# Performance work log

Hardware: AMD Instinct MI355X
Metric: run time of the kernel (lower is better)

The kernel has to match this reference:

```python
import jax, jax.numpy as jnp
import numpy as np

N_NODES = 10000
N_EDGES = 160000
C = 64        # latent channels
H = 512       # MLP hidden width
L = 2         # allegro layers
NB = 8        # bessel basis size
CUT = 2.0     # radial cutoff
AVG = 3.0     # avg_num_neighbors


def setup_inputs() -> dict:
    key = jax.random.key(0)
    ks = jax.random.split(key, 12)
    positions = jax.random.normal(ks[0], (N_NODES, 3), jnp.float32)
    species = jax.random.randint(ks[1], (N_NODES,), 0, 2, jnp.int32)
    senders = jax.random.randint(ks[2], (N_EDGES,), 0, N_NODES, jnp.int32)
    receivers = jax.random.randint(ks[3], (N_EDGES,), 0, N_NODES, jnp.int32)
    w = lambda k, shape, fan: (jax.random.normal(k, shape, jnp.float32) / np.sqrt(fan).astype(np.float32))
    return dict(
        positions=positions,
        W_emb1=w(ks[4], (NB + 4, H), NB + 4),
        W_emb2=w(ks[5], (H, C), H),
        W_v=w(ks[6], (C, C), C),
        W_env=w(ks[7], (L, C, C), C),
        W_lat1=w(ks[8], (L, 3 * C, H), 3 * C),
        W_lat2=w(ks[9], (L, H, C), H),
        W_mix=w(ks[10], (L, C, 2 * C), C),
        W_out=w(ks[11], (C,), C),
        species=species, senders=senders, receivers=receivers,
    )


def reference(positions, W_emb1, W_emb2, W_v, W_env, W_lat1, W_lat2, W_mix, W_out,
              species, senders, receivers):
    node_attrs = jax.nn.one_hot(species, 2, dtype=positions.dtype)   # [N,2]
    r = positions[receivers] - positions[senders]                    # [E,3] edge vectors ('1o')
    d = jnp.sqrt(jnp.sum(r * r, axis=-1))                            # [E]
    dsafe = jnp.maximum(d, 1e-6)
    u = r / dsafe[:, None]                                           # unit vectors = l=1 spherical harmonics

    # radial basis: Bessel functions with smooth polynomial cutoff envelope
    xc = d / CUT
    env = jnp.where(xc < 1.0, (1.0 - xc ** 2) ** 2, 0.0)             # [E]
    nvec = jnp.arange(1, NB + 1, dtype=positions.dtype)
    bessel = jnp.sqrt(2.0 / CUT) * jnp.sin(nvec * jnp.pi * xc[:, None]) / dsafe[:, None]
    rad = bessel * env[:, None]                                      # [E,NB]

    # two-body latent embedding
    feat = jnp.concatenate([rad, node_attrs[senders], node_attrs[receivers]], axis=-1)  # [E,NB+4]
    x = (jax.nn.silu(feat @ W_emb1) @ W_emb2) * env[:, None]         # [E,C]
    # initial equivariant edge features (C channels of 1o)
    V = (x @ W_v)[:, :, None] * u[:, None, :]                        # [E,C,3]

    inv_sqrt2 = 1.0 / jnp.sqrt(2.0)
    for l in range(L):
        # environment density: scatter edge basis to sender nodes, gather back per edge
        w_e = x @ W_env[l]                                           # [E,C]
        rho1 = jax.ops.segment_sum(w_e[:, :, None] * u[:, None, :], senders,
                                   num_segments=N_NODES) / AVG       # [N,C,3] (1o density)
        rho0 = jax.ops.segment_sum(w_e, senders, num_segments=N_NODES) / AVG  # [N,C] (0e density)
        rho1_e = rho1[senders]                                       # [E,C,3]
        rho0_e = rho0[senders]                                       # [E,C]

        # channel-wise Clebsch-Gordan tensor products (lmax=1 paths)
        tp_scal = jnp.einsum('eci,eci->ec', V, rho1_e)               # 1o x 1o -> 0e
        tp_vec1 = V * rho0_e[:, :, None]                             # 1o x 0e -> 1o
        tp_vec2 = jnp.cross(V, rho1_e)                               # 1o x 1o -> 1e

        # latent update (residual, envelope-gated)
        lat_in = jnp.concatenate([x, tp_scal, rho0_e], axis=-1)      # [E,3C]
        dx = (jax.nn.silu(lat_in @ W_lat1[l]) @ W_lat2[l]) * env[:, None]
        x = (x + dx) * inv_sqrt2

        # equivariant update: latent-conditioned mix of tensor-product outputs
        mix = x @ W_mix[l]                                           # [E,2C]
        V = mix[:, :C, None] * tp_vec1 + mix[:, C:, None] * tp_vec2  # [E,C,3]

    # per-edge scalar readout, scatter-reduced to nodes
    e_edge = (x @ W_out) * env                                       # [E]
    node_energy = jax.ops.segment_sum(e_edge, receivers, num_segments=N_NODES) / AVG
    return node_energy
```

## Files before the change

### kernel.cpp

```cpp
#include <hip/hip_runtime.h>
#include <hip/hip_bf16.h>

#define E_NUM 160000
#define NN 10000
#define PI_F 3.14159265358979323846f

using u16 = unsigned short;
using u32 = unsigned int;
typedef short bf16x8 __attribute__((ext_vector_type(8)));
typedef float f32x4 __attribute__((ext_vector_type(4)));
typedef u32 u32x4 __attribute__((ext_vector_type(4)));

__device__ __forceinline__ float silu_fast(float z) {
    return z * __builtin_amdgcn_rcpf(1.0f + __expf(-z));
}
__device__ __forceinline__ float bfb2f(u32 bits16) {
    return __builtin_bit_cast(float, bits16 << 16);
}
__device__ __forceinline__ u32 f2bfb(float f) {
    return (u32)__builtin_bit_cast(u16, __float2bfloat16(f));
}
__device__ __forceinline__ u32 pack2(float lo, float hi) {
    return f2bfb(lo) | (f2bfb(hi) << 16);
}

__global__ void k_detect(const u16* __restrict__ posraw, int* __restrict__ flag) {
    int i = blockIdx.x * 256 + threadIdx.x;
    if (i >= 15000) return;
    float v = bfb2f((u32)posraw[2 * i]);
    if (!(fabsf(v) < 1e4f)) atomicOr(flag, 1);
}

__global__ void k_cvt_all(const void* s0, const void* s1, const void* s2,
                          const void* s3, const void* s4, const void* s5,
                          const void* s6, const void* s7, const void* s8,
                          float* __restrict__ dst, const int* __restrict__ flag) {
    int i = blockIdx.x * 256 + threadIdx.x;
    if (i >= 359792) return;
    const void* src; int off;
    if      (i < 30000)  { src = s0; off = i; }
    else if (i < 36144)  { src = s1; off = i - 30000; }
    else if (i < 68912)  { src = s2; off = i - 36144; }
    else if (i < 73008)  { src = s3; off = i - 68912; }
    else if (i < 81200)  { src = s4; off = i - 73008; }
    else if (i < 277808) { src = s5; off = i - 81200; }
    else if (i < 343344) { src = s6; off = i - 277808; }
    else if (i < 359728) { src = s7; off = i - 343344; }
    else                 { src = s8; off = i - 359728; }
    if (*flag) dst[i] = ((const float*)src)[off];
    else       dst[i] = bfb2f((u32)((const u16*)src)[off]);
}

__global__ void k_pack(const float* __restrict__ W, int K, int Nshift,
                       u16* __restrict__ hi, u16* __restrict__ lo) {
    int i = blockIdx.x * 256 + threadIdx.x;
    int total = K << Nshift;
    if (i >= total) return;
    int k = i >> Nshift, n = i & ((1 << Nshift) - 1);
    float w = W[i];
    u16 h = (u16)f2bfb(w);
    float r = w - bfb2f((u32)h);
    int idx = ((((k >> 3) << Nshift) + n) << 3) + (k & 7);
    hi[idx] = h; lo[idx] = (u16)f2bfb(r);
}

__global__ void k_pack_emb1(const float* __restrict__ W , u16* __restrict__ pk) {
    int i = blockIdx.x * 256 + threadIdx.x;
    if (i >= 64 * 512) return;
    int k = i >> 9, n = i & 511;
    u16 out = 0;
    if (k < 24) {
        out = (u16)f2bfb(W[(k % 12) * 512 + n]);
    } else if (k < 36) {
        float w = W[(k - 24) * 512 + n];
        u16 h = (u16)f2bfb(w);
        out = (u16)f2bfb(w - bfb2f((u32)h));
    }
    pk[((((k >> 3) << 9) + n) << 3) + (k & 7)] = out;
}

__global__ void k_hist(const int* __restrict__ senders, int* __restrict__ counts) {
    int e = blockIdx.x * 256 + threadIdx.x;
    if (e < E_NUM) atomicAdd(&counts[senders[e]], 1);
}

__global__ __launch_bounds__(1024) void k_scan(const int* __restrict__ counts,
                                               int* __restrict__ rowstart) {
    __shared__ int part[1024];
    int t = threadIdx.x;
    int base = t * 10;
    int local[10];
    int sum = 0;
    #pragma unroll
    for (int i = 0; i < 10; i++) {
        int v = (base + i < NN) ? counts[base + i] : 0;
        local[i] = sum; sum += v;
    }
    part[t] = sum;
    __syncthreads();
    for (int off = 1; off < 1024; off <<= 1) {
        int v = (t >= off) ? part[t - off] : 0;
        __syncthreads();
        part[t] += v;
        __syncthreads();
    }
    int pre = (t == 0) ? 0 : part[t - 1];
    #pragma unroll
    for (int i = 0; i < 10; i++)
        if (base + i < NN) rowstart[base + i] = pre + local[i];
    if (t == 1023) rowstart[NN] = part[1023];
}

__global__ void k_copy_int(const int* __restrict__ src, int* __restrict__ dst, int n) {
    int i = blockIdx.x * 256 + threadIdx.x;
    if (i < n) dst[i] = src[i];
}

__global__ void k_fill(const int* __restrict__ senders, int* __restrict__ cursor,
                       int* __restrict__ edge_list) {
    int e = blockIdx.x * 256 + threadIdx.x;
    if (e >= E_NUM) return;
    int pos = atomicAdd(&cursor[senders[e]], 1);
    edge_list[pos] = e;
}

__global__ void k_geom(const float* __restrict__ posf, const int* __restrict__ species,
                       const int* __restrict__ senders, const int* __restrict__ receivers,
                       const int* __restrict__ edge_list,
                       int* __restrict__ ssend, int* __restrict__ srecv,
                       float* __restrict__ ux, float* __restrict__ uy, float* __restrict__ uz,
                       float* __restrict__ envb, u32* __restrict__ latin) {
    int e = blockIdx.x * 256 + threadIdx.x;
    if (e >= E_NUM) return;
    int orig = edge_list[e];
    int s = senders[orig], r = receivers[orig];
    ssend[e] = s; srecv[e] = r;
    float rx = posf[3 * r + 0] - posf[3 * s + 0];
    float ry = posf[3 * r + 1] - posf[3 * s + 1];
    float rz = posf[3 * r + 2] - posf[3 * s + 2];
    float d = sqrtf(rx * rx + ry * ry + rz * rz);
    float inv = 1.0f / fmaxf(d, 1e-6f);
    ux[e] = rx * inv; uy[e] = ry * inv; uz[e] = rz * inv;
    float xc = d * 0.5f;
    float env = 0.0f;
    if (xc < 1.0f) { float t = 1.0f - xc * xc; env = t * t; }
    envb[e] = env;
    float ft[12];
    float se = env * inv;
    #pragma unroll
    for (int n = 1; n <= 8; n++) ft[n - 1] = __sinf((float)n * PI_F * xc) * se;
    int ss = species[s], sr = species[r];
    ft[8] = (ss == 0) ? 1.0f : 0.0f;
    ft[9] = (ss == 1) ? 1.0f : 0.0f;
    ft[10] = (sr == 0) ? 1.0f : 0.0f;
    ft[11] = (sr == 1) ? 1.0f : 0.0f;
    u32 fh[12]; float fl[12];
    #pragma unroll
    for (int i = 0; i < 12; i++) {
        fh[i] = f2bfb(ft[i]);
        fl[i] = ft[i] - bfb2f(fh[i]);
    }
    #pragma unroll
    for (int j = 0; j < 6; j++) {
        u32 v = fh[2 * j] | (fh[2 * j + 1] << 16);
        latin[(size_t)j * E_NUM + e] = v;
        latin[(size_t)(12 + j) * E_NUM + e] = v;
        latin[(size_t)(6 + j) * E_NUM + e] = pack2(fl[2 * j], fl[2 * j + 1]);
    }
}

__global__ __launch_bounds__(256) void k_rho_gather(
    const float* __restrict__ we, const int* __restrict__ rowstart,
    const float* __restrict__ ux, const float* __restrict__ uy,
    const float* __restrict__ uz,
    float* __restrict__ rho0, float* __restrict__ rho1) {
    int wv = (blockIdx.x * 256 + threadIdx.x) >> 6;
    int c = threadIdx.x & 63;
    if (wv >= NN) return;
    int start = rowstart[wv], end = rowstart[wv + 1];
    float s0 = 0.0f, sx = 0.0f, sy = 0.0f, sz = 0.0f;
    for (int j = start; j < end; j++) {
        float w = we[(size_t)j * 64 + c];
        float a = ux[j], b = uy[j], g = uz[j];
        s0 += w;
        sx = fmaf(w, a, sx);
        sy = fmaf(w, b, sy);
        sz = fmaf(w, g, sz);
    }
    const float inv3 = 1.0f / 3.0f;
    rho0[(size_t)wv * 64 + c] = s0 * inv3;
    rho1[(size_t)wv * 192 + 3 * c + 0] = sx * inv3;
    rho1[(size_t)wv * 192 + 3 * c + 1] = sy * inv3;
    rho1[(size_t)wv * 192 + 3 * c + 2] = sz * inv3;
}

template<int KSTEPS, int MODE, int HASLO, int FUSEWE, int STAGE>
__global__ __launch_bounds__(512, 4) void k_mlp(
    const u32* __restrict__ latin,
    const u16* __restrict__ W1hi, const u16* __restrict__ W1lo,
    const u16* __restrict__ W2hi, const u16* __restrict__ W2lo,
    const float* __restrict__ envb,
    u16* __restrict__ xout,
    const u16* __restrict__ wehi, const u16* __restrict__ welo,
    float* __restrict__ webuf,
    const u16* __restrict__ xin,
    const u16* __restrict__ x0t,
    const int* __restrict__ ssend,
    const float* __restrict__ ux, const float* __restrict__ uy,
    const float* __restrict__ uz,
    const float* __restrict__ rho0A, const float* __restrict__ rho1A,
    const float* __restrict__ rho0B, const float* __restrict__ rho1B,
    const u16* __restrict__ wvhi, const u16* __restrict__ wvlo,
    const u16* __restrict__ wmhi, const u16* __restrict__ wmlo) {
    constexpr int ROWDW = KSTEPS * 16;
    constexpr int INAREG = 24576;
    constexpr int SMEMSZ = (STAGE == 2) ? (INAREG + 2 * 16640) : (INAREG + 16640);
    __shared__ __align__(16) char smem[SMEMSZ];
    u32* inA = (u32*)smem;
    u16* hA  = (u16*)(smem + INAREG);
    float* tbA = (float*)(smem + INAREG);
    u16* mb   = (u16*)(smem + INAREG + 16640);
    u32* mb32 = (u32*)(smem + INAREG + 16640);
    u32* xt0  = (u32*)(smem + INAREG + 16640);
    int lane = threadIdx.x & 63;
    int sub = threadIdx.x >> 6;
    int w = __builtin_amdgcn_readfirstlane(sub);
    int l15 = lane & 15, quad = lane >> 4;
    int e0 = blockIdx.x * 64;
    int e = e0 + lane;

    if (STAGE == 0) {
        constexpr int CPW = (KSTEPS * 4) / 8;
        #pragma unroll
        for (int j = 0; j < CPW; j++) {
            int c = w * CPW + j;
            u32x4 v;
            #pragma unroll
            for (int i = 0; i < 4; i++) v[i] = latin[(size_t)(c * 4 + i) * E_NUM + e];
            int slot = (c & ~7) | ((c ^ lane) & 7);
            *(u32x4*)(&inA[lane * ROWDW + slot * 4]) = v;
        }
        __syncthreads();
    } else {
        {
            int c = w;
            u32x4 v;
            #pragma unroll
            for (int i = 0; i < 4; i++) {
                u32 lo = (u32)xin[(size_t)(8 * c + 2 * i) * E_NUM + e];
                u32 hi = (u32)xin[(size_t)(8 * c + 2 * i + 1) * E_NUM + e];
                v[i] = lo | (hi << 16);
            }
            int slot = (c & ~7) | ((c ^ lane) & 7);
            *(u32x4*)(&inA[lane * ROWDW + slot * 4]) = v;
        }
        if (STAGE == 2) {
            int c = w;
            u32x4 v;
            #pragma unroll
            for (int i = 0; i < 4; i++) {
                u32 lo = (u32)x0t[(size_t)(8 * c + 2 * i) * E_NUM + e];
                u32 hi = (u32)x0t[(size_t)(8 * c + 2 * i + 1) * E_NUM + e];
                v[i] = lo | (hi << 16);
            }
            int slot = (c ^ lane) & 7;
            *(u32x4*)(&xt0[lane * 32 + slot * 4]) = v;
        }
        __syncthreads();
        int mt = w & 3;
        int ntbA = (w >> 2) * 2;
        f32x4 accA[2];
        accA[0] = (f32x4){0.f, 0.f, 0.f, 0.f};
        accA[1] = (f32x4){0.f, 0.f, 0.f, 0.f};
        #pragma unroll
        for (int ks = 0; ks < 2; ks++) {
            int c = ks * 4 + quad;
            int m = mt * 16 + l15;
            bf16x8 af;
            if (STAGE == 1) {
                int slot = (c & ~7) | ((c ^ m) & 7);
                af = *(const bf16x8*)(&inA[m * ROWDW + slot * 4]);
            } else {
                int slot = (c ^ m) & 7;
                af = *(const bf16x8*)(&xt0[m * 32 + slot * 4]);
            }
            #pragma unroll
            for (int nti = 0; nti < 2; nti++) {
                int n = (ntbA + nti) * 16 + l15;
                size_t bidx = (((size_t)c << 6) + n) << 3;
                bf16x8 bh = *(const bf16x8*)(wvhi + bidx);
                accA[nti] = __builtin_amdgcn_mfma_f32_16x16x32_bf16(af, bh, accA[nti], 0, 0, 0);
                bf16x8 bl = *(const bf16x8*)(wvlo + bidx);
                accA[nti] = __builtin_amdgcn_mfma_f32_16x16x32_bf16(af, bl, accA[nti], 0, 0, 0);
            }
        }
        f32x4 accM[4];
        if (STAGE == 2) {
            #pragma unroll
            for (int i = 0; i < 4; i++) accM[i] = (f32x4){0.f, 0.f, 0.f, 0.f};
            int nbM = (w >> 2) * 4;
            #pragma unroll
            for (int ks = 0; ks < 2; ks++) {
                int c = ks * 4 + quad;
                int m = mt * 16 + l15;
                int slot = (c & ~7) | ((c ^ m) & 7);
                bf16x8 af = *(const bf16x8*)(&inA[m * ROWDW + slot * 4]);
                #pragma unroll
                for (int nti = 0; nti < 4; nti++) {
                    int n = (nbM + nti) * 16 + l15;
                    size_t bidx = (((size_t)c << 7) + n) << 3;
                    bf16x8 bh = *(const bf16x8*)(wmhi + bidx);
                    accM[nti] = __builtin_amdgcn_mfma_f32_16x16x32_bf16(af, bh, accM[nti], 0, 0, 0);
                    bf16x8 bl = *(const bf16x8*)(wmlo + bidx);
                    accM[nti] = __builtin_amdgcn_mfma_f32_16x16x32_bf16(af, bl, accM[nti], 0, 0, 0);
                }
            }
        }
        __syncthreads();
        #pragma unroll
        for (int nti = 0; nti < 2; nti++) {
            #pragma unroll
            for (int r = 0; r < 4; r++) {
                int rowD = mt * 16 + quad * 4 + r;
                int colD = (ntbA + nti) * 16 + l15;
                tbA[colD * 65 + rowD] = accA[nti][r];
            }
        }
        if (STAGE == 2) {
            int sel = (w >= 4) ? 1 : 0;
            #pragma unroll
            for (int nti = 0; nti < 4; nti++) {
                #pragma unroll
                for (int r = 0; r < 4; r++) {
                    int rowD = mt * 16 + quad * 4 + r;
                    int colD = nti * 16 + l15;
                    mb[((colD * 65 + rowD) << 1) + sel] = (u16)f2bfb(accM[nti][r]);
                }
            }
        }
        __syncthreads();
        int c0 = w * 8;
        float av[8], m1v[8], m2v[8];
        #pragma unroll
        for (int i = 0; i < 8; i++) av[i] = tbA[(c0 + i) * 65 + lane];
        if (STAGE == 2) {
            #pragma unroll
            for (int i = 0; i < 8; i++) {
                u32 pv = mb32[(c0 + i) * 65 + lane];
                m1v[i] = bfb2f(pv & 0xffffu);
                m2v[i] = bfb2f(pv >> 16);
            }
        }
        int s = ssend[e];
        float u0 = ux[e], u1 = uy[e], u2 = uz[e];
        float ts[8], rr[8];
        if (STAGE == 1) {
            const float* r1 = rho1A + (size_t)s * 192;
            const float* r0 = rho0A + (size_t)s * 64;
            #pragma unroll
            for (int i = 0; i < 8; i++) {
                int c = c0 + i;
                float dot = u0 * r1[3 * c] + u1 * r1[3 * c + 1] + u2 * r1[3 * c + 2];
                ts[i] = av[i] * dot;
                rr[i] = r0[c];
            }
        } else {
            const float* r1A = rho1A + (size_t)s * 192;
            const float* r0A = rho0A + (size_t)s * 64;
            const float* r1B = rho1B + (size_t)s * 192;
            const float* r0B = rho0B + (size_t)s * 64;
            #pragma unroll
            for (int i = 0; i < 8; i++) {
                int c = c0 + i;
                float v0 = av[i] * u0, v1 = av[i] * u1, v2 = av[i] * u2;
                float aA0 = r1A[3 * c], aA1 = r1A[3 * c + 1], aA2 = r1A[3 * c + 2];
                float rc = r0A[c];
                float w0 = m1v[i] * v0 * rc + m2v[i] * (v1 * aA2 - v2 * aA1);
                float w1 = m1v[i] * v1 * rc + m2v[i] * (v2 * aA0 - v0 * aA2);
                float w2 = m1v[i] * v2 * rc + m2v[i] * (v0 * aA1 - v1 * aA0);
                ts[i] = w0 * r1B[3 * c] + w1 * r1B[3 * c + 1] + w2 * r1B[3 * c + 2];
                rr[i] = r0B[c];
            }
        }
        u32x4 tv, rv;
        #pragma unroll
        for (int j = 0; j < 4; j++) {
            tv[j] = pack2(ts[2 * j], ts[2 * j + 1]);
            rv[j] = pack2(rr[2 * j], rr[2 * j + 1]);
        }
        {
            int c = 8 + w;
            int slot = (c & ~7) | ((c ^ lane) & 7);
            *(u32x4*)(&inA[lane * ROWDW + slot * 4]) = tv;
        }
        {
            int c = 16 + w;
            int slot = (c & ~7) | ((c ^ lane) & 7);
            *(u32x4*)(&inA[lane * ROWDW + slot * 4]) = rv;
        }
        __syncthreads();
    }

    f32x4 acc2[2];
    acc2[0] = (f32x4){0.f, 0.f, 0.f, 0.f};
    acc2[1] = (f32x4){0.f, 0.f, 0.f, 0.f};
    int nt2 = w & 3;
    int mt2a = (w >> 2) * 2;

    #pragma unroll
    for (int hh = 0; hh < 4; hh++) {
        f32x4 acc[4];
        #pragma unroll
        for (int mt = 0; mt < 4; mt++) acc[mt] = (f32x4){0.f, 0.f, 0.f, 0.f};
        #pragma unroll
        for (int ks = 0; ks < KSTEPS; ks++) {
            int c = ks * 4 + quad;
            bf16x8 afr[4];
            #pragma unroll
            for (int mt = 0; mt < 4; mt++) {
                int m = mt * 16 + l15;
                int slot = (c & ~7) | ((c ^ m) & 7);
                afr[mt] = *(const bf16x8*)(&inA[m * ROWDW + slot * 4]);
            }
            int n = hh * 128 + w * 16 + l15;
            size_t bidx = (((size_t)c << 9) + n) << 3;
            bf16x8 bh = *(const bf16x8*)(W1hi + bidx);
            #pragma unroll
            for (int mt = 0; mt < 4; mt++)
                acc[mt] = __builtin_amdgcn_mfma_f32_16x16x32_bf16(afr[mt], bh, acc[mt], 0, 0, 0);
            if (HASLO) {
                bf16x8 bl = *(const bf16x8*)(W1lo + bidx);
                #pragma unroll
                for (int mt = 0; mt < 4; mt++)
                    acc[mt] = __builtin_amdgcn_mfma_f32_16x16x32_bf16(afr[mt], bl, acc[mt], 0, 0, 0);
            }
        }
        __syncthreads();
        {
            int kh = w * 16 + l15;
            int c = kh >> 3;
            #pragma unroll
            for (int mt = 0; mt < 4; mt++) {
                #pragma unroll
                for (int r = 0; r < 4; r++) {
                    int m = mt * 16 + quad * 4 + r;
                    float s = silu_fast(acc[mt][r]);
                    int slot = (c & 8) | ((c ^ m) & 7);
                    hA[m * 128 + slot * 8 + (kh & 7)] = (u16)f2bfb(s);
                }
            }
        }
        __syncthreads();
        #pragma unroll
        for (int ks = 0; ks < 4; ks++) {
            int c = ks * 4 + quad;
            int m0 = mt2a * 16 + l15;
            int m1i = m0 + 16;
            int s0 = (c & 8) | ((c ^ m0) & 7);
            int s1 = (c & 8) | ((c ^ m1i) & 7);
            bf16x8 a0 = *(const bf16x8*)(&hA[m0 * 128 + s0 * 8]);
            bf16x8 a1 = *(const bf16x8*)(&hA[m1i * 128 + s1 * 8]);
            size_t bidx = (((size_t)(hh * 16 + c) << 6) + nt2 * 16 + l15) << 3;
            bf16x8 bh = *(const bf16x8*)(W2hi + bidx);
            acc2[0] = __builtin_amdgcn_mfma_f32_16x16x32_bf16(a0, bh, acc2[0], 0, 0, 0);
            acc2[1] = __builtin_amdgcn_mfma_f32_16x16x32_bf16(a1, bh, acc2[1], 0, 0, 0);
            bf16x8 bl = *(const bf16x8*)(W2lo + bidx);
            acc2[0] = __builtin_amdgcn_mfma_f32_16x16x32_bf16(a0, bl, acc2[0], 0, 0, 0);
            acc2[1] = __builtin_amdgcn_mfma_f32_16x16x32_bf16(a1, bl, acc2[1], 0, 0, 0);
        }
    }
    float xo[8];
    if (MODE) {
        int c = w;
        int slot = (c & ~7) | ((c ^ lane) & 7);
        #pragma unroll
        for (int i = 0; i < 4; i++) {
            u32 pv = inA[lane * ROWDW + slot * 4 + i];
            xo[2 * i]     = bfb2f(pv & 0xffffu);
            xo[2 * i + 1] = bfb2f(pv >> 16);
        }
    }
    __syncthreads();
    float* epi = (float*)inA;
    #pragma unroll
    for (int mi = 0; mi < 2; mi++) {
        #pragma unroll
        for (int r = 0; r < 4; r++) {
            int m = (mt2a + mi) * 16 + quad * 4 + r;
            int c = nt2 * 16 + l15;
            epi[c * 65 + m] = acc2[mi][r];
        }
    }
    __syncthreads();
    float env = envb[e];
    const float is2 = 0.70710678118654752f;
    #pragma unroll
    for (int i = 0; i < 8; i++) {
        int c = w * 8 + i;
        float v = epi[c * 65 + lane];
        float res;
        if (MODE) res = (xo[i] + v * env) * is2;
        else      res = v * env;
        xout[(size_t)c * E_NUM + e] = (u16)f2bfb(res);
        if (FUSEWE) epi[c * 65 + lane] = res;
    }
    if (FUSEWE) {
        __syncthreads();
        int mt = w & 3;
        int ntb = (w >> 2) * 2;
        f32x4 accw[2];
        accw[0] = (f32x4){0.f, 0.f, 0.f, 0.f};
        accw[1] = (f32x4){0.f, 0.f, 0.f, 0.f};
        #pragma unroll
        for (int ks = 0; ks < 2; ks++) {
            bf16x8 af;
            #pragma unroll
            for (int j = 0; j < 8; j++)
                af[j] = (short)f2bfb(epi[(ks * 32 + quad * 8 + j) * 65 + mt * 16 + l15]);
            #pragma unroll
            for (int nti = 0; nti < 2; nti++) {
                int n4 = (ntb + nti) * 16 + l15;
                size_t bidx = (((size_t)(ks * 4 + quad) << 6) + n4) << 3;
                bf16x8 bh = *(const bf16x8*)(wehi + bidx);
                accw[nti] = __builtin_amdgcn_mfma_f32_16x16x32_bf16(af, bh, accw[nti], 0, 0, 0);
                bf16x8 bl = *(const bf16x8*)(welo + bidx);
                accw[nti] = __builtin_amdgcn_mfma_f32_16x16x32_bf16(af, bl, accw[nti], 0, 0, 0);
            }
        }
        #pragma unroll
        for (int nti = 0; nti < 2; nti++) {
            #pragma unroll
            for (int r = 0; r < 4; r++) {
                int rowD = mt * 16 + quad * 4 + r;
                int colD = (ntb + nti) * 16 + l15;
                webuf[(size_t)(e0 + rowD) * 64 + colD] = accw[nti][r];
            }
        }
    }
}

__global__ void k_readout(const u16* __restrict__ x, const float* __restrict__ Wout,
                          const float* __restrict__ envb, const int* __restrict__ srecv,
                          float* __restrict__ node_acc) {
    int e = blockIdx.x * 256 + threadIdx.x;
    if (e >= E_NUM) return;
    float a = 0.0f;
    #pragma unroll
    for (int c = 0; c < 64; c++) {
        a = fmaf(bfb2f((u32)x[(size_t)c * E_NUM + e]), Wout[c], a);
    }
    a *= envb[e] * (1.0f / 3.0f);
    atomicAdd(&node_acc[srecv[e]], a);
}

__global__ void k_out(const float* __restrict__ node_acc, void* __restrict__ out,
                      const int* __restrict__ flag) {
    int n = blockIdx.x * 256 + threadIdx.x;
    if (n >= NN) return;
    float v = node_acc[n];
    if (*flag) ((float*)out)[n] = v;
    else       ((u16*)out)[n] = (u16)f2bfb(v);
}

extern "C" void kernel_launch(void* const* d_in, const int* in_sizes, int n_in,
                              void* d_out, int out_size, void* d_ws, size_t ws_size,
                              hipStream_t stream) {
    const void* posr   = d_in[0];
    const void* Wemb1r = d_in[1];
    const void* Wemb2r = d_in[2];
    const void* Wvr    = d_in[3];
    const void* Wenvr  = d_in[4];
    const void* Wlat1r = d_in[5];
    const void* Wlat2r = d_in[6];
    const void* Wmixr  = d_in[7];
    const void* Woutr  = d_in[8];
    const int* species   = (const int*)d_in[9];
    const int* senders   = (const int*)d_in[10];
    const int* receivers = (const int*)d_in[11];

    char* p = (char*)d_ws;
    auto alloc = [&](size_t bytes) -> void* {
        void* rp = (void*)p;
        p += (bytes + 255) & ~(size_t)255;
        return rp;
    };
    int*   flag  = (int*)alloc(4);
    float* wbuf  = (float*)alloc(359792 * 4);
    float* posf  = wbuf;
    float* Wemb1 = wbuf + 30000;
    float* Wemb2 = wbuf + 36144;
    float* Wv    = wbuf + 68912;
    float* Wenv  = wbuf + 73008;
    float* Wlat1 = wbuf + 81200;
    float* Wlat2 = wbuf + 277808;
    float* Wmix  = wbuf + 343344;
    float* Wout  = wbuf + 359728;
    const size_t E = E_NUM;
    float* ux   = (float*)alloc(E * 4);
    float* uy   = (float*)alloc(E * 4);
    float* uz   = (float*)alloc(E * 4);
    float* envb = (float*)alloc(E * 4);
    float* rho0A = (float*)alloc((size_t)NN * 64 * 4);
    float* rho1A = (float*)alloc((size_t)NN * 192 * 4);
    float* rho0B = (float*)alloc((size_t)NN * 64 * 4);
    float* rho1B = (float*)alloc((size_t)NN * 192 * 4);
    float* node_acc = (float*)alloc((size_t)NN * 4);
    int* counts    = (int*)alloc((size_t)NN * 4);
    int* rowstart  = (int*)alloc((size_t)(NN + 1) * 4);
    int* cursor    = (int*)alloc((size_t)NN * 4);
    int* edge_list = (int*)alloc(E * 4);
    int* ssend     = (int*)alloc(E * 4);
    int* srecv     = (int*)alloc(E * 4);
    void* unionbuf = alloc(96 * E * 4);
    u32*   latin = (u32*)unionbuf;
    float* webuf = (float*)unionbuf + (size_t)32 * E;
    u16* x0 = (u16*)alloc(64 * E * 2);
    u16* x1 = (u16*)alloc(64 * E * 2);
    u16* w1hi = (u16*)alloc(2 * 98304 * 2);
    u16* w1lo = (u16*)alloc(2 * 98304 * 2);
    u16* w2hi = (u16*)alloc(2 * 32768 * 2);
    u16* w2lo = (u16*)alloc(2 * 32768 * 2);
    u16* e1hi = (u16*)alloc(32768 * 2);
    u16* e2hi = (u16*)alloc(32768 * 2);
    u16* e2lo = (u16*)alloc(32768 * 2);
    u16* we0hi = (u16*)alloc(4096 * 2);
    u16* we0lo = (u16*)alloc(4096 * 2);
    u16* we1hi = (u16*)alloc(4096 * 2);
    u16* we1lo = (u16*)alloc(4096 * 2);
    u16* wvhi  = (u16*)alloc(4096 * 2);
    u16* wvlo  = (u16*)alloc(4096 * 2);
    u16* wmhi  = (u16*)alloc(8192 * 2);
    u16* wmlo  = (u16*)alloc(8192 * 2);

    hipMemsetAsync(flag, 0, 4, stream);
    hipMemsetAsync(counts, 0, (size_t)NN * 4, stream);
    hipMemsetAsync(node_acc, 0, (size_t)NN * 4, stream);
    hipMemsetAsync(latin + (size_t)18 * E, 0, (size_t)14 * E * 4, stream);

    k_detect<<<(15000 + 255) / 256, 256, 0, stream>>>((const u16*)posr, flag);

    k_cvt_all<<<(359792 + 255) / 256, 256, 0, stream>>>(
        posr, Wemb1r, Wemb2r, Wvr, Wenvr, Wlat1r, Wlat2r, Wmixr, Woutr,
        wbuf, flag);

    k_pack_emb1<<<128, 256, 0, stream>>>(Wemb1, e1hi);
    k_pack<<<128, 256, 0, stream>>>(Wemb2, 512, 6, e2hi, e2lo);
    k_pack<<<16, 256, 0, stream>>>(Wenv, 64, 6, we0hi, we0lo);
    k_pack<<<16, 256, 0, stream>>>(Wenv + 4096, 64, 6, we1hi, we1lo);
    k_pack<<<16, 256, 0, stream>>>(Wv, 64, 6, wvhi, wvlo);
    k_pack<<<32, 256, 0, stream>>>(Wmix, 64, 7, wmhi, wmlo);
    for (int l = 0; l < 2; l++) {
        k_pack<<<384, 256, 0, stream>>>(Wlat1 + l * 98304, 192, 9,
                                        w1hi + l * 98304, w1lo + l * 98304);
        k_pack<<<128, 256, 0, stream>>>(Wlat2 + l * 32768, 512, 6,
                                        w2hi + l * 32768, w2lo + l * 32768);
    }

    k_hist<<<625, 256, 0, stream>>>(senders, counts);
    k_scan<<<1, 1024, 0, stream>>>(counts, rowstart);
    k_copy_int<<<(NN + 255) / 256, 256, 0, stream>>>(rowstart, cursor, NN);
    k_fill<<<625, 256, 0, stream>>>(senders, cursor, edge_list);

    k_geom<<<625, 256, 0, stream>>>(posf, species, senders, receivers, edge_list,
                                    ssend, srecv, ux, uy, uz, envb, latin);
    k_mlp<2, 0, 0, 1, 0><<<2500, 512, 0, stream>>>(
        latin, e1hi, nullptr, e2hi, e2lo, envb, x0, we0hi, we0lo, webuf,
        nullptr, nullptr, nullptr, nullptr, nullptr, nullptr,
        nullptr, nullptr, nullptr, nullptr, nullptr, nullptr, nullptr, nullptr);

    k_rho_gather<<<2500, 256, 0, stream>>>(webuf, rowstart, ux, uy, uz,
                                           rho0A, rho1A);
    k_mlp<6, 1, 1, 1, 1><<<2500, 512, 0, stream>>>(
        nullptr, w1hi, w1lo, w2hi, w2lo, envb, x1, we1hi, we1lo, webuf,
        x0, nullptr, ssend, ux, uy, uz, rho0A, rho1A, nullptr, nullptr,
        wvhi, wvlo, nullptr, nullptr);

    k_rho_gather<<<2500, 256, 0, stream>>>(webuf, rowstart, ux, uy, uz,
                                           rho0B, rho1B);
    k_mlp<6, 1, 1, 0, 2><<<2500, 512, 0, stream>>>(
        nullptr, w1hi + 98304, w1lo + 98304, w2hi + 32768, w2lo + 32768,
        envb, x1, nullptr, nullptr, nullptr,
        x1, x0, ssend, ux, uy, uz, rho0A, rho1A, rho0B, rho1B,
        wvhi, wvlo, wmhi, wmlo);

    k_readout<<<625, 256, 0, stream>>>(x1, Wout, envb, srecv, node_acc);
    k_out<<<(NN + 255) / 256, 256, 0, stream>>>(node_acc, d_out, flag);
}
```

Before: 497.8 us.

## Shrink MLP kernel LDS with XOR-swizzled transpose buffers and raise occupancy hint

Replaces the padded stride-65 transpose buffers with an XOR-swizzled 64-stride layout. This lets the scalar and mix buffers share one 16 KB region, with extra barriers so they are used one after the other, and sizes the input region by KSTEPS. Shared memory per block shrinks, and launch bounds now ask for 8 blocks per CU instead of 4 to raise occupancy. The tighter launch bound caps registers per thread and may cause spills, and the added barriers serialize the STAGE 2 epilogue.

Measured after the change: 733.7 us. +47.4%, slower.

```diff
diff --git a/kernel.cpp b/kernel.cpp
--- a/kernel.cpp
+++ b/kernel.cpp
@@ -22,6 +22,9 @@
 }
 __device__ __forceinline__ u32 pack2(float lo, float hi) {
     return f2bfb(lo) | (f2bfb(hi) << 16);
+}
+__device__ __forceinline__ int tbix(int col, int row) {
+    return (col << 6) | (row ^ (col & 31));
 }
 
 __global__ void k_detect(const u16* __restrict__ posraw, int* __restrict__ flag) {
@@ -195,7 +198,7 @@
 }
 
 template<int KSTEPS, int MODE, int HASLO, int FUSEWE, int STAGE>
-__global__ __launch_bounds__(512, 4) void k_mlp(
+__global__ __launch_bounds__(512, 8) void k_mlp(
     const u32* __restrict__ latin,
     const u16* __restrict__ W1hi, const u16* __restrict__ W1lo,
     const u16* __restrict__ W2hi, const u16* __restrict__ W2lo,
@@ -213,15 +216,15 @@
     const u16* __restrict__ wvhi, const u16* __restrict__ wvlo,
     const u16* __restrict__ wmhi, const u16* __restrict__ wmlo) {
     constexpr int ROWDW = KSTEPS * 16;
-    constexpr int INAREG = 24576;
-    constexpr int SMEMSZ = (STAGE == 2) ? (INAREG + 2 * 16640) : (INAREG + 16640);
+    constexpr int INAREG = (KSTEPS * 4096 > 16384) ? (KSTEPS * 4096) : 16384;
+    constexpr int SMEMSZ = INAREG + 16384;
     __shared__ __align__(16) char smem[SMEMSZ];
     u32* inA = (u32*)smem;
     u16* hA  = (u16*)(smem + INAREG);
-    float* tbA = (float*)(smem + INAREG);
-    u16* mb   = (u16*)(smem + INAREG + 16640);
-    u32* mb32 = (u32*)(smem + INAREG + 16640);
-    u32* xt0  = (u32*)(smem + INAREG + 16640);
+    float* tbF = (float*)(smem + INAREG);
+    u16* mb   = (u16*)(smem + INAREG);
+    u32* mb32 = (u32*)(smem + INAREG);
+    u32* xt0  = (u32*)(smem + INAREG);
     int lane = threadIdx.x & 63;
     int sub = threadIdx.x >> 6;
     int w = __builtin_amdgcn_readfirstlane(sub);
@@ -323,10 +326,16 @@
             for (int r = 0; r < 4; r++) {
                 int rowD = mt * 16 + quad * 4 + r;
                 int colD = (ntbA + nti) * 16 + l15;
-                tbA[colD * 65 + rowD] = accA[nti][r];
-            }
-        }
+                tbF[tbix(colD, rowD)] = accA[nti][r];
+            }
+        }
+        __syncthreads();
+        int c0 = w * 8;
+        float av[8], m1v[8], m2v[8];
+        #pragma unroll
+        for (int i = 0; i < 8; i++) av[i] = tbF[tbix(c0 + i, lane)];
         if (STAGE == 2) {
+            __syncthreads();
             int sel = (w >= 4) ? 1 : 0;
             #pragma unroll
             for (int nti = 0; nti < 4; nti++) {
@@ -334,19 +343,13 @@
                 for (int r = 0; r < 4; r++) {
                     int rowD = mt * 16 + quad * 4 + r;
                     int colD = nti * 16 + l15;
-                    mb[((colD * 65 + rowD) << 1) + sel] = (u16)f2bfb(accM[nti][r]);
+                    mb[(tbix(colD, rowD) << 1) + sel] = (u16)f2bfb(accM[nti][r]);
                 }
             }
-        }
-        __syncthreads();
-        int c0 = w * 8;
-        float av[8], m1v[8], m2v[8];
-        #pragma unroll
-        for (int i = 0; i < 8; i++) av[i] = tbA[(c0 + i) * 65 + lane];
-        if (STAGE == 2) {
+            __syncthreads();
             #pragma unroll
             for (int i = 0; i < 8; i++) {
-                u32 pv = mb32[(c0 + i) * 65 + lane];
+                u32 pv = mb32[tbix(c0 + i, lane)];
                 m1v[i] = bfb2f(pv & 0xffffu);
                 m2v[i] = bfb2f(pv >> 16);
             }
@@ -488,7 +491,7 @@
         for (int r = 0; r < 4; r++) {
             int m = (mt2a + mi) * 16 + quad * 4 + r;
             int c = nt2 * 16 + l15;
-            epi[c * 65 + m] = acc2[mi][r];
+            epi[tbix(c, m)] = acc2[mi][r];
         }
     }
     __syncthreads();
@@ -497,12 +500,12 @@
     #pragma unroll
     for (int i = 0; i < 8; i++) {
         int c = w * 8 + i;
-        float v = epi[c * 65 + lane];
+        float v = epi[tbix(c, lane)];
         float res;
         if (MODE) res = (xo[i] + v * env) * is2;
         else      res = v * env;
         xout[(size_t)c * E_NUM + e] = (u16)f2bfb(res);
-        if (FUSEWE) epi[c * 65 + lane] = res;
+        if (FUSEWE) epi[tbix(c, lane)] = res;
     }
     if (FUSEWE) {
         __syncthreads();
@@ -516,7 +519,7 @@
             bf16x8 af;
             #pragma unroll
             for (int j = 0; j < 8; j++)
-                af[j] = (short)f2bfb(epi[(ks * 32 + quad * 8 + j) * 65 + mt * 16 + l15]);
+                af[j] = (short)f2bfb(epi[tbix(ks * 32 + quad * 8 + j, mt * 16 + l15)]);
             #pragma unroll
             for (int nti = 0; nti < 2; nti++) {
                 int n4 = (ntb + nti) * 16 + l15;
```
